# Optimization experiments

Measured on AMD Instinct MI355X. Metric: run time of the kernel, lower is better.

The kernel has to match this reference:

```python
import jax, jax.numpy as jnp
import numpy as np

B, T, D_IN, H, NH, R = 32, 1024, 64, 128, 4, 3
HD = H // NH  # 32


def _p(key, shape, scale=0.02):
    return jax.random.normal(key, shape, dtype=jnp.float32) * scale


def setup_inputs() -> dict:
    key = jax.random.key(0)
    ks = jax.random.split(key, 8)
    return {
        "x": jax.random.normal(ks[0], (B, T, D_IN), dtype=jnp.float32),
        "theta_w": _p(ks[1], (H, D_IN)),
        "theta_b": jnp.zeros((H,), jnp.float32),
        "in_proj_w": _p(ks[2], (3 * H, H)),
        "in_proj_b": jnp.zeros((3 * H,), jnp.float32),
        "out_proj_w": _p(ks[3], (H, H)),
        "out_proj_b": jnp.zeros((H,), jnp.float32),
        "ln_g": jnp.ones((H,), jnp.float32),
        "ln_b": jnp.zeros((H,), jnp.float32),
        "w1": _p(ks[4], (H, H)),
        "b1": jnp.zeros((H,), jnp.float32),
        "w2": _p(ks[5], (2, H)),
        "b2": jnp.zeros((2,), jnp.float32),
    }


def _build_adj(t, radius):
    # banded adjacency: adj[i,j] = 1/(1+|i-j|) for |i-j| <= radius, row-normalized
    idx = jnp.arange(t)
    d = jnp.abs(idx[:, None] - idx[None, :])
    adj = jnp.where(d <= radius, 1.0 / (1.0 + d.astype(jnp.float32)), 0.0)
    return adj / jnp.clip(adj.sum(axis=1, keepdims=True), 1e-8)


def reference(x, theta_w, theta_b, in_proj_w, in_proj_b, out_proj_w, out_proj_b,
              ln_g, ln_b, w1, b1, w2, b2):
    h = x @ theta_w.T + theta_b                       # [B,T,H]
    adj = _build_adj(T, R)                            # [T,T]
    g = jnp.einsum('ij,bjh->bih', adj, h)             # banded temporal aggregation

    # torch nn.MultiheadAttention (batch_first, eval -> no dropout)
    qkv = g @ in_proj_w.T + in_proj_b                 # [B,T,3H]
    q, k, v = jnp.split(qkv, 3, axis=-1)
    split_heads = lambda t: t.reshape(B, T, NH, HD).transpose(0, 2, 1, 3)
    q, k, v = split_heads(q), split_heads(k), split_heads(v)
    scores = jnp.einsum('bntd,bnsd->bnts', q, k) / jnp.sqrt(jnp.float32(HD))
    attn = jax.nn.softmax(scores, axis=-1)
    o = jnp.einsum('bnts,bnsd->bntd', attn, v)
    o = o.transpose(0, 2, 1, 3).reshape(B, T, H)
    a = o @ out_proj_w.T + out_proj_b                 # [B,T,H]

    # head on last timestep: LayerNorm -> Linear -> GELU(exact) -> Linear
    last = a[:, -1, :]                                # [B,H]
    mu = last.mean(-1, keepdims=True)
    var = ((last - mu) ** 2).mean(-1, keepdims=True)
    ln = (last - mu) / jnp.sqrt(var + 1e-5) * ln_g + ln_b
    hid = jax.nn.gelu(ln @ w1.T + b1, approximate=False)
    return hid @ w2.T + b2                            # [B,2]
```

## Files before the change

### kernel.cpp

```cpp
#include <hip/hip_runtime.h>
#include <math.h>

#define TT 1024

__global__ __launch_bounds__(256) void k_main(
    const float* __restrict__ x, const float* __restrict__ theta_w,
    const float* __restrict__ theta_b, const float* __restrict__ ipw,
    const float* __restrict__ ipb, float* __restrict__ u_p,
    float* __restrict__ d_p) {
  const int b = blockIdx.x >> 4;
  const int c = blockIdx.x & 15;
  const int tid = threadIdx.x;
  const int base = c * 64 - 6;

  __shared__ float s_xs[64];
  __shared__ float s_y[128];
  __shared__ float s_q[128];
  __shared__ float s_z[4][128];
  __shared__ __align__(16) float s_r[256];
  __shared__ __align__(16) float s_x[80 * 64];
  __shared__ float s_t[4][80];
  __shared__ float s_e[4][76];
  __shared__ float s_p[4][76];
  __shared__ float s_pt[4][64];

  const float* __restrict__ xb = x + (size_t)b * TT * 64;
  const int g = tid >> 4, l16 = tid & 15;

  if (tid < 64) {
    float acc = xb[(TT - 1) * 64 + tid]
              + 0.5f        * xb[(TT - 2) * 64 + tid]
              + (1.f / 3.f) * xb[(TT - 3) * 64 + tid]
              + 0.25f       * xb[(TT - 4) * 64 + tid];
    s_xs[tid] = acc * (12.f / 25.f);
  }
  __syncthreads();
  for (int pass = 0; pass < 8; ++pass) {
    const int e = pass * 16 + g;
    const float4 wv = *(const float4*)(theta_w + e * 64 + l16 * 4);
    const float* xs4 = &s_xs[l16 * 4];
    float acc = wv.x * xs4[0] + wv.y * xs4[1] + wv.z * xs4[2] + wv.w * xs4[3];
    acc += __shfl_xor(acc, 1); acc += __shfl_xor(acc, 2);
    acc += __shfl_xor(acc, 4); acc += __shfl_xor(acc, 8);
    if (l16 == 0) s_y[e] = acc + theta_b[e];
  }
  __syncthreads();
  for (int pass = 0; pass < 8; ++pass) {
    const int e = pass * 16 + g;
    const float* wr = ipw + e * 128 + l16 * 8;
    const float* yy = &s_y[l16 * 8];
    float acc = 0.f;
    #pragma unroll
    for (int u = 0; u < 8; ++u) acc += wr[u] * yy[u];
    acc += __shfl_xor(acc, 1); acc += __shfl_xor(acc, 2);
    acc += __shfl_xor(acc, 4); acc += __shfl_xor(acc, 8);
    if (l16 == 0) s_q[e] = acc + ipb[e];
  }
  __syncthreads();
  for (int rep = 0; rep < 2; ++rep) {
    const int idx = tid + rep * 256;
    const int n = idx >> 7, cc = idx & 127;
    const float* qn = &s_q[n * 32];
    float acc = 0.f;
    for (int e = 0; e < 32; ++e) acc += ipw[(128 + n * 32 + e) * 128 + cc] * qn[e];
    s_z[n][cc] = acc;
  }
  __syncthreads();
  {
    const int n = tid >> 6, d = tid & 63;
    const float* zn = s_z[n];
    float acc = 0.f;
    for (int cc = 0; cc < 128; ++cc) acc += theta_w[cc * 64 + d] * zn[cc];
    s_r[n * 64 + d] = acc * 0.17677669529663687f;
  }
  __syncthreads();

  #pragma unroll
  for (int it = 0; it < 5; ++it) {
    const int i4 = tid + it * 256;
    const int ri = i4 >> 4;
    const int j = base + ri;
    float4 v = make_float4(0.f, 0.f, 0.f, 0.f);
    if (j >= 0 && j < TT) v = ((const float4*)(xb + (size_t)j * 64))[i4 & 15];
    ((float4*)s_x)[i4] = v;
  }
  __syncthreads();
  {
    const float4 r0 = ((const float4*)(s_r +   0))[l16];
    const float4 r1 = ((const float4*)(s_r +  64))[l16];
    const float4 r2 = ((const float4*)(s_r + 128))[l16];
    const float4 r3 = ((const float4*)(s_r + 192))[l16];
    for (int it = 0; it < 5; ++it) {
      const int ri = it * 16 + g;
      const float4 xv = ((const float4*)(s_x + ri * 64))[l16];
      float p0 = xv.x * r0.x + xv.y * r0.y + xv.z * r0.z + xv.w * r0.w;
      float p1 = xv.x * r1.x + xv.y * r1.y + xv.z * r1.z + xv.w * r1.w;
      float p2 = xv.x * r2.x + xv.y * r2.y + xv.z * r2.z + xv.w * r2.w;
      float p3 = xv.x * r3.x + xv.y * r3.y + xv.z * r3.z + xv.w * r3.w;
      #pragma unroll
      for (int m = 1; m <= 8; m <<= 1) {
        p0 += __shfl_xor(p0, m);
        p1 += __shfl_xor(p1, m);
        p2 += __shfl_xor(p2, m);
        p3 += __shfl_xor(p3, m);
      }
      if (l16 == 0) {
        s_t[0][ri] = p0; s_t[1][ri] = p1; s_t[2][ri] = p2; s_t[3][ri] = p3;
      }
    }
  }
  __syncthreads();

  const int n = tid >> 6, l = tid & 63;
  #pragma unroll
  for (int rnd = 0; rnd < 2; ++rnd) {
    const int sl = (rnd == 0) ? (l + 3) : (l + 67);
    if (rnd == 0 || l < 6) {
      const int s = base + sl;
      float e_val = 0.f, p_val = 0.f;
      if (s >= 0 && s < TT) {
        float acc = 0.f, wsum = 0.f;
        #pragma unroll
        for (int dj = -3; dj <= 3; ++dj) {
          const int j = s + dj;
          if (j >= 0 && j < TT) {
            const float w = 1.f / (1.f + (float)(dj < 0 ? -dj : dj));
            acc += w * s_t[n][sl + dj];
            wsum += w;
          }
        }
        e_val = expf(acc / wsum);
        p_val = e_val / wsum;
      }
      s_e[n][sl] = e_val;
      s_p[n][sl] = p_val;
    }
  }
  __syncthreads();
  {
    float ev = s_e[n][6 + l];
    #pragma unroll
    for (int m = 32; m >= 1; m >>= 1) ev += __shfl_xor(ev, m);
    if (l == 0) d_p[blockIdx.x * 4 + n] = ev;
  }
  {
    float acc = 0.f;
    #pragma unroll
    for (int dj = -3; dj <= 3; ++dj)
      acc += (1.f / (1.f + (float)(dj < 0 ? -dj : dj))) * s_p[n][6 + l + dj];
    s_pt[n][l] = acc;
  }
  __syncthreads();
  {
    float acc = 0.f;
    #pragma unroll 8
    for (int k = 0; k < 64; ++k)
      acc += s_pt[n][k] * s_x[(k + 6) * 64 + l];
    u_p[(size_t)blockIdx.x * 256 + n * 64 + l] = acc;
  }
}

__global__ __launch_bounds__(256) void k_tail(
    const float* __restrict__ u_p, const float* __restrict__ d_p,
    const float* __restrict__ theta_w, const float* __restrict__ theta_b,
    const float* __restrict__ ipw, const float* __restrict__ ipb,
    const float* __restrict__ Wout, const float* __restrict__ outb,
    const float* __restrict__ ln_g, const float* __restrict__ ln_b,
    const float* __restrict__ w1, const float* __restrict__ b1,
    const float* __restrict__ w2, const float* __restrict__ b2,
    float* __restrict__ out) {
  const int b = blockIdx.x;
  const int tid = threadIdx.x;
  __shared__ float s_u[256];
  __shared__ float s_w[4][128];
  __shared__ float s_o[128], s_a[128], s_ln[128], s_hid[128], s_red[2];
  __shared__ float s_dn[4];

  if (tid < 64) {
    const int n = tid >> 4, cc = tid & 15;
    float v = d_p[(b * 16 + cc) * 4 + n];
    v += __shfl_xor(v, 1); v += __shfl_xor(v, 2);
    v += __shfl_xor(v, 4); v += __shfl_xor(v, 8);
    if (cc == 0) s_dn[n] = v;
  }
  __syncthreads();
  {
    const int n = tid >> 6;
    float acc = 0.f;
    for (int cc = 0; cc < 16; ++cc)
      acc += u_p[(size_t)(b * 16 + cc) * 256 + tid];
    s_u[tid] = acc / s_dn[n];
  }
  __syncthreads();

  const int g = tid >> 4, l16 = tid & 15;
  for (int pass = 0; pass < 32; ++pass) {
    const int o = pass * 16 + g;
    const int n = o >> 7, cc = o & 127;
    const float4 wv = *(const float4*)(theta_w + cc * 64 + l16 * 4);
    const float* un = &s_u[n * 64 + l16 * 4];
    float acc = wv.x * un[0] + wv.y * un[1] + wv.z * un[2] + wv.w * un[3];
    acc += __shfl_xor(acc, 1); acc += __shfl_xor(acc, 2);
    acc += __shfl_xor(acc, 4); acc += __shfl_xor(acc, 8);
    if (l16 == 0) s_w[n][cc] = acc + theta_b[cc];
  }
  __syncthreads();
  for (int pass = 0; pass < 8; ++pass) {
    const int e = pass * 16 + g;
    const float* wr = ipw + (256 + e) * 128 + l16 * 8;
    const float* wn = &s_w[e >> 5][l16 * 8];
    float acc = 0.f;
    #pragma unroll
    for (int u = 0; u < 8; ++u) acc += wr[u] * wn[u];
    acc += __shfl_xor(acc, 1); acc += __shfl_xor(acc, 2);
    acc += __shfl_xor(acc, 4); acc += __shfl_xor(acc, 8);
    if (l16 == 0) s_o[e] = acc + ipb[256 + e];
  }
  __syncthreads();
  for (int pass = 0; pass < 8; ++pass) {
    const int e = pass * 16 + g;
    const float* wr = Wout + e * 128 + l16 * 8;
    const float* oo = &s_o[l16 * 8];
    float acc = 0.f;
    #pragma unroll
    for (int u = 0; u < 8; ++u) acc += wr[u] * oo[u];
    acc += __shfl_xor(acc, 1); acc += __shfl_xor(acc, 2);
    acc += __shfl_xor(acc, 4); acc += __shfl_xor(acc, 8);
    if (l16 == 0) s_a[e] = acc + outb[e];
  }
  __syncthreads();
  const float a = (tid < 128) ? s_a[tid] : 0.f;
  float sum = a;
  #pragma unroll
  for (int m = 32; m >= 1; m >>= 1) sum += __shfl_xor(sum, m);
  if (tid == 0) s_red[0] = sum;
  if (tid == 64) s_red[1] = sum;
  __syncthreads();
  const float mu = (s_red[0] + s_red[1]) * (1.f / 128.f);
  __syncthreads();
  const float dv = (tid < 128) ? (a - mu) : 0.f;
  float sq = dv * dv;
  #pragma unroll
  for (int m = 32; m >= 1; m >>= 1) sq += __shfl_xor(sq, m);
  if (tid == 0) s_red[0] = sq;
  if (tid == 64) s_red[1] = sq;
  __syncthreads();
  const float var = (s_red[0] + s_red[1]) * (1.f / 128.f);
  if (tid < 128)
    s_ln[tid] = dv / sqrtf(var + 1e-5f) * ln_g[tid] + ln_b[tid];
  __syncthreads();
  for (int pass = 0; pass < 8; ++pass) {
    const int e = pass * 16 + g;
    const float* wr = w1 + e * 128 + l16 * 8;
    const float* ll = &s_ln[l16 * 8];
    float acc = 0.f;
    #pragma unroll
    for (int u = 0; u < 8; ++u) acc += wr[u] * ll[u];
    acc += __shfl_xor(acc, 1); acc += __shfl_xor(acc, 2);
    acc += __shfl_xor(acc, 4); acc += __shfl_xor(acc, 8);
    if (l16 == 0) {
      float h = acc + b1[e];
      s_hid[e] = 0.5f * h * (1.f + erff(h * 0.70710678118654752f));
    }
  }
  __syncthreads();
  if (g < 2) {
    const float* wr = w2 + g * 128 + l16 * 8;
    const float* hh = &s_hid[l16 * 8];
    float acc = 0.f;
    #pragma unroll
    for (int u = 0; u < 8; ++u) acc += wr[u] * hh[u];
    acc += __shfl_xor(acc, 1); acc += __shfl_xor(acc, 2);
    acc += __shfl_xor(acc, 4); acc += __shfl_xor(acc, 8);
    if (l16 == 0) out[b * 2 + g] = acc + b2[g];
  }
}

extern "C" void kernel_launch(void* const* d_in, const int* in_sizes, int n_in,
                              void* d_out, int out_size, void* d_ws, size_t ws_size,
                              hipStream_t stream) {
  const float* x       = (const float*)d_in[0];
  const float* theta_w = (const float*)d_in[1];
  const float* theta_b = (const float*)d_in[2];
  const float* ipw     = (const float*)d_in[3];
  const float* ipb     = (const float*)d_in[4];
  const float* outw    = (const float*)d_in[5];
  const float* outb    = (const float*)d_in[6];
  const float* ln_g    = (const float*)d_in[7];
  const float* ln_b    = (const float*)d_in[8];
  const float* w1      = (const float*)d_in[9];
  const float* b1      = (const float*)d_in[10];
  const float* w2      = (const float*)d_in[11];
  const float* b2      = (const float*)d_in[12];

  float* ws  = (float*)d_ws;
  float* u_p = ws;
  float* d_p = ws + 131072;

  k_main<<<512, 256, 0, stream>>>(x, theta_w, theta_b, ipw, ipb, u_p, d_p);
  k_tail<<< 32, 256, 0, stream>>>(u_p, d_p, theta_w, theta_b, ipw, ipb,
                                  outw, outb, ln_g, ln_b, w1, b1, w2, b2,
                                  (float*)d_out);
}
```

Measured before the change: 122.6 us.

## Split per-batch query precompute into separate kernel and keep x tile in registers

Moves the last-timestep query/r-vector computation, which was redundantly recomputed by all 16 chunk blocks of each batch, into a new 32-block kernel that writes r to workspace. The main kernel now holds its x rows in registers instead of a 20 KB shared tile, and computes the final weighted sum as per-group partials reduced through shared memory. This removes redundant weight reads and shared traffic but adds a kernel launch and a global round-trip for r.

New measurement: 123.3 us. No clear change (+0.5%).

```diff
diff --git a/kernel.cpp b/kernel.cpp
--- a/kernel.cpp
+++ b/kernel.cpp
@@ -3,27 +3,16 @@
 
 #define TT 1024
 
-__global__ __launch_bounds__(256) void k_main(
+__global__ __launch_bounds__(256) void k_qr(
     const float* __restrict__ x, const float* __restrict__ theta_w,
     const float* __restrict__ theta_b, const float* __restrict__ ipw,
-    const float* __restrict__ ipb, float* __restrict__ u_p,
-    float* __restrict__ d_p) {
-  const int b = blockIdx.x >> 4;
-  const int c = blockIdx.x & 15;
+    const float* __restrict__ ipb, float* __restrict__ r_out) {
+  const int b = blockIdx.x;
   const int tid = threadIdx.x;
-  const int base = c * 64 - 6;
-
   __shared__ float s_xs[64];
   __shared__ float s_y[128];
   __shared__ float s_q[128];
   __shared__ float s_z[4][128];
-  __shared__ __align__(16) float s_r[256];
-  __shared__ __align__(16) float s_x[80 * 64];
-  __shared__ float s_t[4][80];
-  __shared__ float s_e[4][76];
-  __shared__ float s_p[4][76];
-  __shared__ float s_pt[4][64];
-
   const float* __restrict__ xb = x + (size_t)b * TT * 64;
   const int g = tid >> 4, l16 = tid & 15;
 
@@ -71,32 +60,51 @@
     const float* zn = s_z[n];
     float acc = 0.f;
     for (int cc = 0; cc < 128; ++cc) acc += theta_w[cc * 64 + d] * zn[cc];
-    s_r[n * 64 + d] = acc * 0.17677669529663687f;
-  }
-  __syncthreads();
-
+    r_out[(b * 4 + n) * 64 + d] = acc * 0.17677669529663687f;
+  }
+}
+
+__global__ __launch_bounds__(256) void k_main(
+    const float* __restrict__ x, const float* __restrict__ r_in,
+    float* __restrict__ u_p, float* __restrict__ d_p) {
+  const int b = blockIdx.x >> 4;
+  const int c = blockIdx.x & 15;
+  const int tid = threadIdx.x;
+  const int base = c * 64 - 6;
+  const int g = tid >> 4, l16 = tid & 15;
+
+  __shared__ __align__(16) float s_r[256];
+  __shared__ float s_t[4][80];
+  __shared__ float s_e[4][76];
+  __shared__ float s_p[4][76];
+  __shared__ float s_pt[4][64];
+  __shared__ __align__(16) float s_up[16][256];
+
+  const float* __restrict__ xb = x + (size_t)b * TT * 64;
+
+  float4 xv[5];
   #pragma unroll
   for (int it = 0; it < 5; ++it) {
-    const int i4 = tid + it * 256;
-    const int ri = i4 >> 4;
-    const int j = base + ri;
-    float4 v = make_float4(0.f, 0.f, 0.f, 0.f);
-    if (j >= 0 && j < TT) v = ((const float4*)(xb + (size_t)j * 64))[i4 & 15];
-    ((float4*)s_x)[i4] = v;
-  }
-  __syncthreads();
+    const int j = base + it * 16 + g;
+    xv[it] = make_float4(0.f, 0.f, 0.f, 0.f);
+    if (j >= 0 && j < TT)
+      xv[it] = ((const float4*)(xb + (size_t)j * 64))[l16];
+  }
+  s_r[tid] = r_in[b * 256 + tid];
+  __syncthreads();
+
   {
     const float4 r0 = ((const float4*)(s_r +   0))[l16];
     const float4 r1 = ((const float4*)(s_r +  64))[l16];
     const float4 r2 = ((const float4*)(s_r + 128))[l16];
     const float4 r3 = ((const float4*)(s_r + 192))[l16];
+    #pragma unroll
     for (int it = 0; it < 5; ++it) {
-      const int ri = it * 16 + g;
-      const float4 xv = ((const float4*)(s_x + ri * 64))[l16];
-      float p0 = xv.x * r0.x + xv.y * r0.y + xv.z * r0.z + xv.w * r0.w;
-      float p1 = xv.x * r1.x + xv.y * r1.y + xv.z * r1.z + xv.w * r1.w;
-      float p2 = xv.x * r2.x + xv.y * r2.y + xv.z * r2.z + xv.w * r2.w;
-      float p3 = xv.x * r3.x + xv.y * r3.y + xv.z * r3.z + xv.w * r3.w;
+      const float4 v = xv[it];
+      float p0 = v.x * r0.x + v.y * r0.y + v.z * r0.z + v.w * r0.w;
+      float p1 = v.x * r1.x + v.y * r1.y + v.z * r1.z + v.w * r1.w;
+      float p2 = v.x * r2.x + v.y * r2.y + v.z * r2.z + v.w * r2.w;
+      float p3 = v.x * r3.x + v.y * r3.y + v.z * r3.z + v.w * r3.w;
       #pragma unroll
       for (int m = 1; m <= 8; m <<= 1) {
         p0 += __shfl_xor(p0, m);
@@ -105,6 +113,7 @@
         p3 += __shfl_xor(p3, m);
       }
       if (l16 == 0) {
+        const int ri = it * 16 + g;
         s_t[0][ri] = p0; s_t[1][ri] = p1; s_t[2][ri] = p2; s_t[3][ri] = p3;
       }
     }
@@ -151,12 +160,35 @@
     s_pt[n][l] = acc;
   }
   __syncthreads();
-  {
-    float acc = 0.f;
-    #pragma unroll 8
-    for (int k = 0; k < 64; ++k)
-      acc += s_pt[n][k] * s_x[(k + 6) * 64 + l];
-    u_p[(size_t)blockIdx.x * 256 + n * 64 + l] = acc;
+
+  {
+    float4 un[4];
+    #pragma unroll
+    for (int nn = 0; nn < 4; ++nn) un[nn] = make_float4(0.f, 0.f, 0.f, 0.f);
+    #pragma unroll
+    for (int it = 0; it < 5; ++it) {
+      const int ri = it * 16 + g;
+      if (ri >= 6 && ri < 70) {
+        const int jl = ri - 6;
+        const float4 v = xv[it];
+        #pragma unroll
+        for (int nn = 0; nn < 4; ++nn) {
+          const float pv = s_pt[nn][jl];
+          un[nn].x += pv * v.x; un[nn].y += pv * v.y;
+          un[nn].z += pv * v.z; un[nn].w += pv * v.w;
+        }
+      }
+    }
+    #pragma unroll
+    for (int nn = 0; nn < 4; ++nn)
+      ((float4*)&s_up[g][nn * 64])[l16] = un[nn];
+  }
+  __syncthreads();
+  {
+    float acc = 0.f;
+    #pragma unroll
+    for (int gg = 0; gg < 16; ++gg) acc += s_up[gg][tid];
+    u_p[(size_t)blockIdx.x * 256 + tid] = acc;
   }
 }
 
@@ -294,10 +326,12 @@
   const float* b2      = (const float*)d_in[12];
 
   float* ws  = (float*)d_ws;
-  float* u_p = ws;
-  float* d_p = ws + 131072;
-
-  k_main<<<512, 256, 0, stream>>>(x, theta_w, theta_b, ipw, ipb, u_p, d_p);
+  float* r   = ws;
+  float* u_p = ws + 8192;
+  float* d_p = ws + 8192 + 131072;
+
+  k_qr  <<< 32, 256, 0, stream>>>(x, theta_w, theta_b, ipw, ipb, r);
+  k_main<<<512, 256, 0, stream>>>(x, r, u_p, d_p);
   k_tail<<< 32, 256, 0, stream>>>(u_p, d_p, theta_w, theta_b, ipw, ipb,
                                   outw, outb, ln_g, ln_b, w1, b1, w2, b2,
                                   (float*)d_out);
```
